# Kernel optimization log

Measured on AMD Instinct MI355X. Metric: run time of the kernel, lower is better.

Reference implementation:

```python
import jax, jax.numpy as jnp
import numpy as np

N = 65536            # query points (256x256 image)
G = 2048             # number of gaussian/gabor primitives
K = 8                # top-k wave frequencies per primitive
NUM_TOTAL_FREQ = 128
MAX_FREQ = 128.0


def setup_inputs() -> dict:
    key = jax.random.key(0)
    ks = jax.random.split(key, 7)
    x = jax.random.uniform(ks[0], (N, 2), jnp.float32)
    gaussian_colors = 0.05 * jax.random.normal(ks[1], (G, 3), jnp.float32)
    gaussian_positions = jax.random.uniform(ks[2], (G, 2), jnp.float32)
    gaussian_scales = 3.0 + 0.05 * jax.random.normal(ks[3], (G, 2), jnp.float32)
    gaussian_rotations = jnp.pi * jax.random.uniform(ks[4], (G, 1), jnp.float32)
    topk_wave_coefficients = 0.01 * (2.0 * jax.random.uniform(ks[5], (G, K), jnp.float32) - 1.0)
    topk_wave_indices = jax.random.randint(ks[6], (G, K), 0, NUM_TOTAL_FREQ)
    return {
        "x": x,
        "gaussian_colors": gaussian_colors,
        "gaussian_positions": gaussian_positions,
        "gaussian_scales": gaussian_scales,
        "gaussian_rotations": gaussian_rotations,
        "topk_wave_coefficients": topk_wave_coefficients,
        "topk_wave_indices": topk_wave_indices,
    }


def reference(x, gaussian_colors, gaussian_positions, gaussian_scales,
              gaussian_rotations, topk_wave_coefficients, topk_wave_indices):
    # Dense (unblocked) faithful evaluation of the periodic-primitive splat:
    # out[n] = sum_g color_g * exp(-0.5*((rx*sx)^2+(ry*sy)^2)) * sum_k c_gk*cos(2*pi*f_gk*rx)
    dx = x[:, None, 0] - gaussian_positions[None, :, 0]   # [N, G]
    dy = x[:, None, 1] - gaussian_positions[None, :, 1]   # [N, G]
    th = gaussian_rotations[:, 0]                          # [G]
    c, s = jnp.cos(th), jnp.sin(th)
    rx = c[None, :] * dx + s[None, :] * dy                 # rotated coords [N, G]
    ry = -s[None, :] * dx + c[None, :] * dy
    sx = gaussian_scales[None, :, 0]
    sy = gaussian_scales[None, :, 1]
    env = jnp.exp(-0.5 * ((rx * sx) ** 2 + (ry * sy) ** 2))  # gaussian envelope [N, G]
    # frequency of each selected coefficient: idx * max_freq / num_total_freq
    freqs = topk_wave_indices.astype(jnp.float32) * (MAX_FREQ / NUM_TOTAL_FREQ)  # [G, K]
    two_pi = 2.0 * jnp.pi
    wave = jnp.zeros_like(env)
    for k in range(K):  # small fixed loop -> avoids materializing [N, G, K]
        wave = wave + topk_wave_coefficients[:, k][None, :] * jnp.cos(two_pi * freqs[:, k][None, :] * rx)
    return (env * wave) @ gaussian_colors  # [N, 3]
```

## Files before the change

### kernel.cpp

```cpp
#include <hip/hip_runtime.h>
#include <math.h>

#define G_NUM   2048
#define N_PTS   65536
#define K_FREQ  8
#define REC     64
#define CHUNKS  32
#define G_PER_CHUNK (G_NUM / CHUNKS)
#define PACK_BYTES ((size_t)G_NUM * REC * sizeof(float))
#define PART_FLOATS ((size_t)N_PTS * 3)
#define PART_BYTES  (PART_FLOATS * sizeof(float) * CHUNKS)
#define LDS_FLOATS  (G_PER_CHUNK * REC)

typedef float v2f __attribute__((ext_vector_type(2)));

#if __has_builtin(__builtin_amdgcn_cosf)
__device__ __forceinline__ float hw_cos_rev(float p) { return __builtin_amdgcn_cosf(p); }
#else
__device__ __forceinline__ float hw_cos_rev(float p) { return __cosf(6.28318530717958648f * p); }
#endif
#if __has_builtin(__builtin_amdgcn_exp2f)
__device__ __forceinline__ float hw_exp2(float p) { return __builtin_amdgcn_exp2f(p); }
#else
__device__ __forceinline__ float hw_exp2(float p) { return exp2f(p); }
#endif

__device__ __forceinline__ v2f fma2v(v2f a, v2f b, v2f c) {
#if __has_builtin(__builtin_elementwise_fma)
    return __builtin_elementwise_fma(a, b, c);
#else
    v2f r; r.x = fmaf(a.x, b.x, c.x); r.y = fmaf(a.y, b.y, c.y); return r;
#endif
}

__global__ __launch_bounds__(256) void pack_kernel(
    const float* __restrict__ colors, const float* __restrict__ pos,
    const float* __restrict__ scales, const float* __restrict__ rot,
    const float* __restrict__ coef,   const int* __restrict__ idx,
    float* __restrict__ pack)
{
    int j = blockIdx.x * blockDim.x + threadIdx.x;
    if (j >= G_NUM) return;
    float th = rot[j];
    float c = cosf(th), s = sinf(th);
    float px = pos[2 * j], py = pos[2 * j + 1];
    float sx = scales[2 * j], sy = scales[2 * j + 1];
    const float nhl2e = -0.72134752044448170368f;
    float* r = pack + (size_t)j * REC;
    auto put = [&](int pair, float v) { r[2 * pair] = v; r[2 * pair + 1] = v; };
    put(0, -(c * px + s * py));
    put(1, s * px - c * py);
    put(2, c);
    put(3, s);
    put(4, -s);
    put(5, nhl2e * sx * sx);
    put(6, nhl2e * sy * sy);
    put(7, colors[3 * j]);
    put(8, colors[3 * j + 1]);
    put(9, colors[3 * j + 2]);
#pragma unroll
    for (int k = 0; k < K_FREQ; ++k) {
        put(10 + k, (float)idx[j * K_FREQ + k]);
        put(18 + k, coef[j * K_FREQ + k]);
    }
#pragma unroll
    for (int p = 26; p < 32; ++p) put(p, 0.0f);
}

template <bool USE_PART>
__global__ __launch_bounds__(256, 8) void periodic2d_kernel(
    const float* __restrict__ x, const float* __restrict__ pack,
    float* __restrict__ dst )
{
    __shared__ float lds_rec[LDS_FLOATS];

    {
        const float4* __restrict__ src = (const float4*)
            (pack + (size_t)(blockIdx.y * G_PER_CHUNK) * REC);
        float4* dstl = (float4*)lds_rec;
#pragma unroll
        for (int i = 0; i < LDS_FLOATS / 4 / 256; ++i)
            dstl[threadIdx.x + 256 * i] = src[threadIdx.x + 256 * i];
    }
    __syncthreads();

    const int t = blockIdx.x * 256 + threadIdx.x;
    const int p0 = t;
    const int p1 = t + N_PTS / 4;
    const int p2 = t + N_PTS / 2;
    const int p3 = t + 3 * (N_PTS / 4);
    const float2 q0 = ((const float2*)x)[p0];
    const float2 q1 = ((const float2*)x)[p1];
    const float2 q2 = ((const float2*)x)[p2];
    const float2 q3 = ((const float2*)x)[p3];
    const v2f xiA = {q0.x, q1.x}, yiA = {q0.y, q1.y};
    const v2f xiB = {q2.x, q3.x}, yiB = {q2.y, q3.y};
    v2f a0A = {0.f, 0.f}, a1A = {0.f, 0.f}, a2A = {0.f, 0.f};
    v2f a0B = {0.f, 0.f}, a1B = {0.f, 0.f}, a2B = {0.f, 0.f};

    const v2f* rv = (const v2f*)lds_rec;
#pragma unroll 1
    for (int j = 0; j < G_PER_CHUNK; ++j, rv += REC / 2) {
        const v2f rxA = fma2v(xiA, rv[2], fma2v(yiA, rv[3], rv[0]));
        const v2f rxB = fma2v(xiB, rv[2], fma2v(yiB, rv[3], rv[0]));
        const v2f ryA = fma2v(yiA, rv[2], fma2v(xiA, rv[4], rv[1]));
        const v2f ryB = fma2v(yiB, rv[2], fma2v(xiB, rv[4], rv[1]));
        const v2f eargA = fma2v(ryA * rv[6], ryA, (rxA * rv[5]) * rxA);
        const v2f eargB = fma2v(ryB * rv[6], ryB, (rxB * rv[5]) * rxB);
        v2f envA, envB;
        envA.x = hw_exp2(eargA.x); envA.y = hw_exp2(eargA.y);
        envB.x = hw_exp2(eargB.x); envB.y = hw_exp2(eargB.y);
        v2f waveA = {0.f, 0.f}, waveB = {0.f, 0.f};
#pragma unroll
        for (int k = 0; k < K_FREQ; ++k) {
            const v2f phA = rxA * rv[10 + k];
            const v2f phB = rxB * rv[10 + k];
            v2f cA, cB;
            cA.x = hw_cos_rev(phA.x); cA.y = hw_cos_rev(phA.y);
            cB.x = hw_cos_rev(phB.x); cB.y = hw_cos_rev(phB.y);
            waveA = fma2v(cA, rv[18 + k], waveA);
            waveB = fma2v(cB, rv[18 + k], waveB);
        }
        const v2f wA = envA * waveA;
        const v2f wB = envB * waveB;
        a0A = fma2v(wA, rv[7], a0A);  a0B = fma2v(wB, rv[7], a0B);
        a1A = fma2v(wA, rv[8], a1A);  a1B = fma2v(wB, rv[8], a1B);
        a2A = fma2v(wA, rv[9], a2A);  a2B = fma2v(wB, rv[9], a2B);
    }

    if (USE_PART) {
        float* o = dst + (size_t)blockIdx.y * PART_FLOATS;
        o[3 * p0 + 0] = a0A.x; o[3 * p0 + 1] = a1A.x; o[3 * p0 + 2] = a2A.x;
        o[3 * p1 + 0] = a0A.y; o[3 * p1 + 1] = a1A.y; o[3 * p1 + 2] = a2A.y;
        o[3 * p2 + 0] = a0B.x; o[3 * p2 + 1] = a1B.x; o[3 * p2 + 2] = a2B.x;
        o[3 * p3 + 0] = a0B.y; o[3 * p3 + 1] = a1B.y; o[3 * p3 + 2] = a2B.y;
    } else {
        atomicAdd(&dst[3 * p0 + 0], a0A.x);
        atomicAdd(&dst[3 * p0 + 1], a1A.x);
        atomicAdd(&dst[3 * p0 + 2], a2A.x);
        atomicAdd(&dst[3 * p1 + 0], a0A.y);
        atomicAdd(&dst[3 * p1 + 1], a1A.y);
        atomicAdd(&dst[3 * p1 + 2], a2A.y);
        atomicAdd(&dst[3 * p2 + 0], a0B.x);
        atomicAdd(&dst[3 * p2 + 1], a1B.x);
        atomicAdd(&dst[3 * p2 + 2], a2B.x);
        atomicAdd(&dst[3 * p3 + 0], a0B.y);
        atomicAdd(&dst[3 * p3 + 1], a1B.y);
        atomicAdd(&dst[3 * p3 + 2], a2B.y);
    }
}

__global__ __launch_bounds__(256) void reduce_kernel(
    const float* __restrict__ part, float* __restrict__ out)
{
    const int i = blockIdx.x * 256 + threadIdx.x;
    float4 s = {0.f, 0.f, 0.f, 0.f};
#pragma unroll
    for (int c = 0; c < CHUNKS; ++c) {
        const float4 v = ((const float4*)(part + (size_t)c * PART_FLOATS))[i];
        s.x += v.x; s.y += v.y; s.z += v.z; s.w += v.w;
    }
    ((float4*)out)[i] = s;
}

extern "C" void kernel_launch(void* const* d_in, const int* in_sizes, int n_in,
                              void* d_out, int out_size, void* d_ws, size_t ws_size,
                              hipStream_t stream)
{
    const float* x      = (const float*)d_in[0];
    const float* colors = (const float*)d_in[1];
    const float* pos    = (const float*)d_in[2];
    const float* scales = (const float*)d_in[3];
    const float* rot    = (const float*)d_in[4];
    const float* coef   = (const float*)d_in[5];
    const int*   idx    = (const int*)d_in[6];
    float* out  = (float*)d_out;
    float* pack = (float*)d_ws;
    float* part = (float*)((char*)d_ws + PACK_BYTES);

    pack_kernel<<<dim3((G_NUM + 255) / 256), 256, 0, stream>>>(
        colors, pos, scales, rot, coef, idx, pack);

    if (ws_size >= PACK_BYTES + PART_BYTES) {
        periodic2d_kernel<true><<<dim3(N_PTS / 1024, CHUNKS), 256, 0, stream>>>(
            x, pack, part);
        reduce_kernel<<<dim3((N_PTS * 3 / 4) / 256), 256, 0, stream>>>(part, out);
    } else {
        (void)hipMemsetAsync(d_out, 0, (size_t)out_size * sizeof(float), stream);
        periodic2d_kernel<false><<<dim3(N_PTS / 1024, CHUNKS), 256, 0, stream>>>(
            x, pack, out);
    }
}
```

Before: 201.9 us.

## Replace per-frequency cosines with per-gaussian cubic lookup tables and Morton-sorted points

Each gaussian's wave sum (8 weighted cosines in rx) is precomputed into a 2048-cell cubic-polynomial table over rx in [-1.5, 1.5]. The main kernel then does one table gather plus a cubic evaluation per point-gaussian pair instead of 8 hardware cosines. Query points are bucketed by Morton cell in a single-block sort so that gathers within a wave hit nearby table entries, and the reduction scatters results back through the permutation. This adds a roughly 64 MB table build, a serial single-block sort and random global gathers. Accuracy now depends on interpolating frequencies up to 127 with only a few cells per period, and on rx staying inside the table range.

New measurement: 274.8 us. +36.1%, slower.

```diff
diff --git a/kernel.cpp b/kernel.cpp
--- a/kernel.cpp
+++ b/kernel.cpp
@@ -9,8 +9,20 @@
 #define G_PER_CHUNK (G_NUM / CHUNKS)
 #define PACK_BYTES ((size_t)G_NUM * REC * sizeof(float))
 #define PART_FLOATS ((size_t)N_PTS * 3)
-#define PART_BYTES  (PART_FLOATS * sizeof(float) * CHUNKS)
+#define PART_BYTES_OLD (PART_FLOATS * sizeof(float) * CHUNKS)
 #define LDS_FLOATS  (G_PER_CHUNK * REC)
+
+#define S_TAB   2048
+#define INV_H   (2048.0f / 3.0f)
+#define TAB_BYTES   ((size_t)G_NUM * S_TAB * 16)
+#define XS_BYTES    ((size_t)N_PTS * 8)
+#define PERM_BYTES  ((size_t)N_PTS * 4)
+#define PART4_BYTES ((size_t)CHUNKS * N_PTS * 16)
+#define OFF_TAB   (PACK_BYTES)
+#define OFF_XS    (OFF_TAB + TAB_BYTES)
+#define OFF_PERM  (OFF_XS + XS_BYTES)
+#define OFF_PART4 (OFF_PERM + PERM_BYTES)
+#define NEW_TOTAL (OFF_PART4 + PART4_BYTES)
 
 typedef float v2f __attribute__((ext_vector_type(2)));
 
@@ -70,10 +82,9 @@
 template <bool USE_PART>
 __global__ __launch_bounds__(256, 8) void periodic2d_kernel(
     const float* __restrict__ x, const float* __restrict__ pack,
-    float* __restrict__ dst )
+    float* __restrict__ dst)
 {
     __shared__ float lds_rec[LDS_FLOATS];
-
     {
         const float4* __restrict__ src = (const float4*)
             (pack + (size_t)(blockIdx.y * G_PER_CHUNK) * REC);
@@ -163,6 +174,199 @@
     ((float4*)out)[i] = s;
 }
 
+
+__global__ __launch_bounds__(256) void build_tab_kernel(
+    const float* __restrict__ colors, const float* __restrict__ pos,
+    const float* __restrict__ scales, const float* __restrict__ rot,
+    const float* __restrict__ coef,   const int* __restrict__ idx,
+    float* __restrict__ pack, float* __restrict__ tab)
+{
+    const int g = blockIdx.y;
+    if (blockIdx.x == 0 && threadIdx.x == 0) {
+        float th = rot[g];
+        float c = cosf(th), s = sinf(th);
+        float px = pos[2 * g], py = pos[2 * g + 1];
+        float sx = scales[2 * g], sy = scales[2 * g + 1];
+        const float nhl2e = -0.72134752044448170368f;
+        float* r = pack + (size_t)g * REC;
+        auto put = [&](int pair, float v) { r[2 * pair] = v; r[2 * pair + 1] = v; };
+        put(0, -(c * px + s * py));
+        put(1, s * px - c * py);
+        put(2, c); put(3, s); put(4, -s);
+        put(5, nhl2e * sx * sx);
+        put(6, nhl2e * sy * sy);
+        put(7, colors[3 * g]); put(8, colors[3 * g + 1]); put(9, colors[3 * g + 2]);
+    }
+    const int i = blockIdx.x * 256 + threadIdx.x;
+    float nk[K_FREQ], ck[K_FREQ];
+#pragma unroll
+    for (int k = 0; k < K_FREQ; ++k) {
+        nk[k] = (float)idx[g * K_FREQ + k];
+        ck[k] = coef[g * K_FREQ + k];
+    }
+    float w[4];
+#pragma unroll
+    for (int m = 0; m < 4; ++m) {
+        const float xm = (float)(3 * i + m - 3072) * 0x1p-11f;
+        float acc = 0.f;
+#pragma unroll
+        for (int k = 0; k < K_FREQ; ++k)
+            acc = fmaf(ck[k], hw_cos_rev(nk[k] * xm), acc);
+        w[m] = acc;
+    }
+    const float d1 = w[1] - w[0];
+    const float d2 = w[2] - 2.f * w[1] + w[0];
+    const float d3 = w[3] - 3.f * w[2] + 3.f * w[1] - w[0];
+    float4 o;
+    o.x = w[0];
+    o.y = 3.f * d1 - 1.5f * d2 + d3;
+    o.z = 4.5f * (d2 - d3);
+    o.w = 4.5f * d3;
+    ((float4*)tab)[(size_t)g * S_TAB + i] = o;
+}
+
+__device__ __forceinline__ int cell_id(float px, float py) {
+    int cx = (int)(px * 32.f); cx = cx > 31 ? 31 : cx;
+    int cy = (int)(py * 32.f); cy = cy > 31 ? 31 : cy;
+    int m = 0;
+#pragma unroll
+    for (int b = 0; b < 5; ++b)
+        m |= (((cx >> b) & 1) << (2 * b)) | (((cy >> b) & 1) << (2 * b + 1));
+    return m;
+}
+
+__global__ __launch_bounds__(1024) void sort_kernel(
+    const float* __restrict__ x, float* __restrict__ xs, int* __restrict__ perm)
+{
+    __shared__ int h[1024];
+    __shared__ int e[1024];
+    const int tid = threadIdx.x;
+    h[tid] = 0;
+    __syncthreads();
+    const float4* xv4 = (const float4*)x;
+#pragma unroll 1
+    for (int it = 0; it < N_PTS / 2048; ++it) {
+        const float4 p = xv4[tid + 1024 * it];
+        atomicAdd(&h[cell_id(p.x, p.y)], 1);
+        atomicAdd(&h[cell_id(p.z, p.w)], 1);
+    }
+    __syncthreads();
+    const int v = h[tid];
+    e[tid] = v;
+    __syncthreads();
+#pragma unroll 1
+    for (int d = 1; d < 1024; d <<= 1) {
+        const int a = (tid >= d) ? e[tid - d] : 0;
+        __syncthreads();
+        e[tid] += a;
+        __syncthreads();
+    }
+    h[tid] = e[tid] - v;
+    __syncthreads();
+#pragma unroll 1
+    for (int it = 0; it < N_PTS / 2048; ++it) {
+        const int i0 = 2 * (tid + 1024 * it);
+        const float4 p = xv4[tid + 1024 * it];
+        int pos = atomicAdd(&h[cell_id(p.x, p.y)], 1);
+        ((float2*)xs)[pos] = make_float2(p.x, p.y);
+        perm[pos] = i0;
+        pos = atomicAdd(&h[cell_id(p.z, p.w)], 1);
+        ((float2*)xs)[pos] = make_float2(p.z, p.w);
+        perm[pos] = i0 + 1;
+    }
+}
+
+__global__ __launch_bounds__(256, 8) void periodic2d_tab_kernel(
+    const float* __restrict__ xs, const float* __restrict__ pack,
+    const float* __restrict__ tab, float* __restrict__ part)
+{
+    __shared__ float lds_rec[G_PER_CHUNK * 32];
+    {
+        const float4* __restrict__ src = (const float4*)
+            (pack + (size_t)(blockIdx.y * G_PER_CHUNK) * REC);
+        float4* d4 = (float4*)lds_rec;
+#pragma unroll
+        for (int it = 0; it < 2; ++it) {
+            const int i = threadIdx.x + 256 * it;
+            d4[i] = src[((i >> 3) << 4) | (i & 7)];
+        }
+    }
+    __syncthreads();
+
+    const int t = blockIdx.x * 256 + threadIdx.x;
+    const int p0 = ((t >> 6) << 8) | (t & 63);
+    const float2 q0 = ((const float2*)xs)[p0];
+    const float2 q1 = ((const float2*)xs)[p0 + 64];
+    const float2 q2 = ((const float2*)xs)[p0 + 128];
+    const float2 q3 = ((const float2*)xs)[p0 + 192];
+    const v2f xiA = {q0.x, q1.x}, yiA = {q0.y, q1.y};
+    const v2f xiB = {q2.x, q3.x}, yiB = {q2.y, q3.y};
+    v2f a0A = {0.f, 0.f}, a1A = {0.f, 0.f}, a2A = {0.f, 0.f};
+    v2f a0B = {0.f, 0.f}, a1B = {0.f, 0.f}, a2B = {0.f, 0.f};
+    const v2f vinvh = {INV_H, INV_H};
+    const v2f voff  = {1024.f, 1024.f};
+
+    const v2f* rv = (const v2f*)lds_rec;
+    const float4* __restrict__ tb =
+        (const float4*)tab + (size_t)(blockIdx.y * G_PER_CHUNK) * S_TAB;
+#pragma unroll 1
+    for (int j = 0; j < G_PER_CHUNK; ++j, rv += 16, tb += S_TAB) {
+        const v2f rxA = fma2v(xiA, rv[2], fma2v(yiA, rv[3], rv[0]));
+        const v2f rxB = fma2v(xiB, rv[2], fma2v(yiB, rv[3], rv[0]));
+        const v2f ryA = fma2v(yiA, rv[2], fma2v(xiA, rv[4], rv[1]));
+        const v2f ryB = fma2v(yiB, rv[2], fma2v(xiB, rv[4], rv[1]));
+        const v2f uA = fma2v(rxA, vinvh, voff);
+        const v2f uB = fma2v(rxB, vinvh, voff);
+        const float fA0 = floorf(uA.x), fA1 = floorf(uA.y);
+        const float fB0 = floorf(uB.x), fB1 = floorf(uB.y);
+        const int iA0 = (int)fA0, iA1 = (int)fA1;
+        const int iB0 = (int)fB0, iB1 = (int)fB1;
+        const float4 cA0 = tb[iA0], cA1 = tb[iA1];
+        const float4 cB0 = tb[iB0], cB1 = tb[iB1];
+        const float tA0 = uA.x - fA0, tA1 = uA.y - fA1;
+        const float tB0 = uB.x - fB0, tB1 = uB.y - fB1;
+        v2f wvA, wvB;
+        wvA.x = fmaf(fmaf(fmaf(cA0.w, tA0, cA0.z), tA0, cA0.y), tA0, cA0.x);
+        wvA.y = fmaf(fmaf(fmaf(cA1.w, tA1, cA1.z), tA1, cA1.y), tA1, cA1.x);
+        wvB.x = fmaf(fmaf(fmaf(cB0.w, tB0, cB0.z), tB0, cB0.y), tB0, cB0.x);
+        wvB.y = fmaf(fmaf(fmaf(cB1.w, tB1, cB1.z), tB1, cB1.y), tB1, cB1.x);
+        const v2f eargA = fma2v(ryA * rv[6], ryA, (rxA * rv[5]) * rxA);
+        const v2f eargB = fma2v(ryB * rv[6], ryB, (rxB * rv[5]) * rxB);
+        v2f envA, envB;
+        envA.x = hw_exp2(eargA.x); envA.y = hw_exp2(eargA.y);
+        envB.x = hw_exp2(eargB.x); envB.y = hw_exp2(eargB.y);
+        const v2f wA = envA * wvA;
+        const v2f wB = envB * wvB;
+        a0A = fma2v(wA, rv[7], a0A);  a0B = fma2v(wB, rv[7], a0B);
+        a1A = fma2v(wA, rv[8], a1A);  a1B = fma2v(wB, rv[8], a1B);
+        a2A = fma2v(wA, rv[9], a2A);  a2B = fma2v(wB, rv[9], a2B);
+    }
+
+    float4* o = (float4*)part + (size_t)blockIdx.y * N_PTS;
+    o[p0      ] = make_float4(a0A.x, a1A.x, a2A.x, 0.f);
+    o[p0 +  64] = make_float4(a0A.y, a1A.y, a2A.y, 0.f);
+    o[p0 + 128] = make_float4(a0B.x, a1B.x, a2B.x, 0.f);
+    o[p0 + 192] = make_float4(a0B.y, a1B.y, a2B.y, 0.f);
+}
+
+__global__ __launch_bounds__(256) void reduce_tab_kernel(
+    const float* __restrict__ part, const int* __restrict__ perm,
+    float* __restrict__ out)
+{
+    const int p = blockIdx.x * 256 + threadIdx.x;
+    const float4* p4 = (const float4*)part;
+    float sx = 0.f, sy = 0.f, sz = 0.f;
+#pragma unroll
+    for (int c = 0; c < CHUNKS; ++c) {
+        const float4 v = p4[(size_t)c * N_PTS + p];
+        sx += v.x; sy += v.y; sz += v.z;
+    }
+    const int q = perm[p];
+    out[3 * q    ] = sx;
+    out[3 * q + 1] = sy;
+    out[3 * q + 2] = sz;
+}
+
 extern "C" void kernel_launch(void* const* d_in, const int* in_sizes, int n_in,
                               void* d_out, int out_size, void* d_ws, size_t ws_size,
                               hipStream_t stream)
@@ -176,12 +380,25 @@
     const int*   idx    = (const int*)d_in[6];
     float* out  = (float*)d_out;
     float* pack = (float*)d_ws;
+
+    if (ws_size >= NEW_TOTAL) {
+        float* tab  = (float*)((char*)d_ws + OFF_TAB);
+        float* xs   = (float*)((char*)d_ws + OFF_XS);
+        int*   perm = (int*)  ((char*)d_ws + OFF_PERM);
+        float* part = (float*)((char*)d_ws + OFF_PART4);
+        build_tab_kernel<<<dim3(S_TAB / 256, G_NUM), 256, 0, stream>>>(
+            colors, pos, scales, rot, coef, idx, pack, tab);
+        sort_kernel<<<dim3(1), 1024, 0, stream>>>(x, xs, perm);
+        periodic2d_tab_kernel<<<dim3(N_PTS / 1024, CHUNKS), 256, 0, stream>>>(
+            xs, pack, tab, part);
+        reduce_tab_kernel<<<dim3(N_PTS / 256), 256, 0, stream>>>(part, perm, out);
+        return;
+    }
+
     float* part = (float*)((char*)d_ws + PACK_BYTES);
-
     pack_kernel<<<dim3((G_NUM + 255) / 256), 256, 0, stream>>>(
         colors, pos, scales, rot, coef, idx, pack);
-
-    if (ws_size >= PACK_BYTES + PART_BYTES) {
+    if (ws_size >= PACK_BYTES + PART_BYTES_OLD) {
         periodic2d_kernel<true><<<dim3(N_PTS / 1024, CHUNKS), 256, 0, stream>>>(
             x, pack, part);
         reduce_kernel<<<dim3((N_PTS * 3 / 4) / 256), 256, 0, stream>>>(part, out);
```
